# Kernel optimization log

Hardware: AMD Instinct MI355X
Metric: run time of the kernel (lower is better)

The kernel has to match this reference:

```python
import jax, jax.numpy as jnp
import numpy as np


def _gru_cell(x, h, W_ih, W_hh, b_ih, b_hh):
    # torch.nn.GRUCell math. x: [T,H], h: [T,H]; W_*: [3H,H]; b_*: [3H]
    gi = x @ W_ih.T + b_ih          # [T,3H]
    gh = h @ W_hh.T + b_hh          # [T,3H]
    i_r, i_z, i_n = jnp.split(gi, 3, axis=-1)
    h_r, h_z, h_n = jnp.split(gh, 3, axis=-1)
    r = jax.nn.sigmoid(i_r + h_r)
    z = jax.nn.sigmoid(i_z + h_z)
    n = jnp.tanh(i_n + r * h_n)
    return (1.0 - z) * n + z * h


def setup_inputs() -> dict:
    key = jax.random.key(0)
    ks = jax.random.split(key, 7)
    S, T, H = 65536, 8192, 1024
    bound = 1.0 / np.sqrt(H)  # torch GRUCell init scale
    return {
        "speaker_memory": jax.random.normal(ks[0], (S, H), dtype=jnp.float32),
        "speaker_ids": jax.random.randint(ks[1], (T,), 0, S, dtype=jnp.int32),
        "edu_reps": jax.random.normal(ks[2], (T, H), dtype=jnp.float32),
        "W_ih": jax.random.uniform(ks[3], (3 * H, H), jnp.float32, -bound, bound),
        "W_hh": jax.random.uniform(ks[4], (3 * H, H), jnp.float32, -bound, bound),
        "b_ih": jax.random.uniform(ks[5], (3 * H,), jnp.float32, -bound, bound),
        "b_hh": jax.random.uniform(ks[6], (3 * H,), jnp.float32, -bound, bound),
    }


def reference(speaker_memory, speaker_ids, edu_reps, W_ih, W_hh, b_ih, b_hh):
    # The torch loop reads h from the ORIGINAL speaker_memory for every step,
    # so all T GRU updates are independent; for duplicate speaker ids the last
    S, H = speaker_memory.shape
    T = speaker_ids.shape[0]
    h = speaker_memory[speaker_ids]                      # [T,H] gather
    new_h = _gru_cell(edu_reps, h, W_ih, W_hh, b_ih, b_hh)  # [T,H]
    # last occurrence position of each speaker id (int min for untouched ids)
    last_pos = jax.ops.segment_max(jnp.arange(T), speaker_ids, num_segments=S)
    touched = last_pos >= 0                              # [S]
    gathered = new_h[jnp.clip(last_pos, 0, T - 1)]       # [S,H]
    return jnp.where(touched[:, None], gathered, speaker_memory)
```

## Files before the change

kernel.cpp:

```cpp
#include <hip/hip_runtime.h>
#include <hip/hip_bf16.h>
#include <stdint.h>
#include <stddef.h>

typedef short short8 __attribute__((ext_vector_type(8)));
typedef float f32x4 __attribute__((ext_vector_type(4)));

#define SROWS 65536
#define TROWS 8192
#define HDIM  1024
#define KDIM  2048
#define NDIM  4096
#define NT    (KDIM / 64)

__device__ __forceinline__ unsigned short f2bf(float f) {
  union { float f; uint32_t u; } v; v.f = f;
  uint32_t u = v.u;
  uint32_t r = (u + 0x7FFFu + ((u >> 16) & 1u)) >> 16;
  return (unsigned short)r;
}

__device__ __forceinline__ float fast_sigmoid(float x) {
  return __builtin_amdgcn_rcpf(1.0f + __builtin_amdgcn_exp2f(-1.44269504f * x));
}
__device__ __forceinline__ float fast_tanh(float x) {
  return 1.0f - 2.0f * __builtin_amdgcn_rcpf(1.0f + __builtin_amdgcn_exp2f(2.88539008f * x));
}


__global__ __launch_bounds__(256) void k_initlp(int* lp) {
  int i = blockIdx.x * 256 + threadIdx.x;
  if (i < SROWS) lp[i] = -1;
}

__global__ __launch_bounds__(256) void k_lp(const int* __restrict__ sid, int* lp) {
  int i = blockIdx.x * 256 + threadIdx.x;
  if (i < TROWS) atomicMax(&lp[sid[i]], i);
}

__global__ __launch_bounds__(256) void k_flags(const int* __restrict__ lp,
                                               unsigned long long* __restrict__ flagb) {
  int i = blockIdx.x * 256 + threadIdx.x;
  unsigned long long m = __ballot(lp[i] < 0);
  if ((threadIdx.x & 63) == 0) flagb[i >> 6] = m;
}

__global__ __launch_bounds__(256) void k_bias(const float* __restrict__ bih,
                                              const float* __restrict__ bhh,
                                              float* __restrict__ btab) {
  int j = blockIdx.x * 256 + threadIdx.x;
  if (j < HDIM) {
    btab[4*j+0] = bih[j] + bhh[j];
    btab[4*j+1] = bih[j+HDIM] + bhh[j+HDIM];
    btab[4*j+2] = bih[j+2*HDIM];
    btab[4*j+3] = bhh[j+2*HDIM];
  }
}

__global__ __launch_bounds__(256) void k_build_A(const float* __restrict__ edu,
                                                 const float* __restrict__ mem,
                                                 const int* __restrict__ sid,
                                                 unsigned short* __restrict__ Ac) {
  const int idx = blockIdx.x * 256 + threadIdx.x;
  const int t  = idx >> 8;
  const int k0 = (idx & 255) << 3;
  const float* src;
  if (k0 < HDIM) src = edu + (size_t)t * HDIM + k0;
  else           src = mem + (size_t)sid[t] * HDIM + (k0 - HDIM);
  f32x4 f0 = *(const f32x4*)src;
  f32x4 f1 = *(const f32x4*)(src + 4);
  short8 v;
  v[0]=(short)f2bf(f0[0]); v[1]=(short)f2bf(f0[1]); v[2]=(short)f2bf(f0[2]); v[3]=(short)f2bf(f0[3]);
  v[4]=(short)f2bf(f1[0]); v[5]=(short)f2bf(f1[1]); v[6]=(short)f2bf(f1[2]); v[7]=(short)f2bf(f1[3]);
  *(short8*)(Ac + (size_t)idx * 8) = v;
}

__global__ __launch_bounds__(256) void k_build_B(const float* __restrict__ Wih,
                                                 const float* __restrict__ Whh,
                                                 unsigned short* __restrict__ Bc) {
  const int idx = blockIdx.x * 256 + threadIdx.x;
  const int c  = idx >> 8;
  const int k0 = (idx & 255) << 3;
  const int j  = c >> 2;
  const int g  = c & 3;
  const float* src = nullptr;
  if (g == 0)      src = (k0 < HDIM) ? Wih + (size_t)j * HDIM + k0
                                     : Whh + (size_t)j * HDIM + (k0 - HDIM);
  else if (g == 1) src = (k0 < HDIM) ? Wih + (size_t)(j + HDIM) * HDIM + k0
                                     : Whh + (size_t)(j + HDIM) * HDIM + (k0 - HDIM);
  else if (g == 2) { if (k0 < HDIM)  src = Wih + (size_t)(j + 2*HDIM) * HDIM + k0; }
  else             { if (k0 >= HDIM) src = Whh + (size_t)(j + 2*HDIM) * HDIM + (k0 - HDIM); }
  short8 v = (short8)0;
  if (src) {
    f32x4 f0 = *(const f32x4*)src;
    f32x4 f1 = *(const f32x4*)(src + 4);
    v[0]=(short)f2bf(f0[0]); v[1]=(short)f2bf(f0[1]); v[2]=(short)f2bf(f0[2]); v[3]=(short)f2bf(f0[3]);
    v[4]=(short)f2bf(f1[0]); v[5]=(short)f2bf(f1[1]); v[6]=(short)f2bf(f1[2]); v[7]=(short)f2bf(f1[3]);
  }
  *(short8*)(Bc + (size_t)idx * 8) = v;
}


#define FENCE() asm volatile("" ::: "memory")
#define BAR()   __builtin_amdgcn_s_barrier()
#define LGKM0() asm volatile("s_waitcnt lgkmcnt(0)" ::: "memory")
#define VM(N)   asm volatile("s_waitcnt vmcnt(" #N ")" ::: "memory")

#define STAGE(p0, p1, ldsoff)                                                              \
  __builtin_amdgcn_global_load_lds((const __attribute__((address_space(1))) void*)(p0),   \
      (__attribute__((address_space(3))) void*)(smem + (ldsoff) + w * 1024), 16, 0, 0);    \
  __builtin_amdgcn_global_load_lds((const __attribute__((address_space(1))) void*)(p1),   \
      (__attribute__((address_space(3))) void*)(smem + (ldsoff) + 8192 + w * 1024), 16, 0, 0);

#define LDF(base, frag, koff) (*(const short8*)(smem + (base) + (size_t)(frag) * 2048 + (koff)))

__global__ __launch_bounds__(512, 2)
void k_gru8(const unsigned short* __restrict__ Ac,
            const unsigned short* __restrict__ Bc,
            const float* __restrict__ mem,
            const int* __restrict__ sid,
            const int* __restrict__ lp,
            const unsigned long long* __restrict__ flagb,
            const float* __restrict__ btab,
            float* __restrict__ out) {
  extern __shared__ char smem[];

  const int tid  = threadIdx.x;
  const int lane = tid & 63;
  const int w    = tid >> 6;
  const int wm   = w >> 2;
  const int wn   = w & 3;
  const int l15  = lane & 15;
  const int l4   = lane >> 4;

  const int bid = blockIdx.x;
  const int swz = (bid & 7) * 64 + (bid >> 3);
  const int t0  = (swz >> 4) * 256;
  const int c0  = (swz & 15) * 256;

  const int srow0 = tid >> 3;
  const int srow1 = 64 + srow0;
  const int scol  = ((tid & 7) * 8) ^ (((tid >> 3) & 7) << 3);

  const unsigned short* pA0r0 = Ac + (size_t)(t0 +       srow0) * KDIM + scol;
  const unsigned short* pA0r1 = Ac + (size_t)(t0 +       srow1) * KDIM + scol;
  const unsigned short* pA1r0 = Ac + (size_t)(t0 + 128 + srow0) * KDIM + scol;
  const unsigned short* pA1r1 = Ac + (size_t)(t0 + 128 + srow1) * KDIM + scol;
  const unsigned short* pB0r0 = Bc + (size_t)(c0 +       srow0) * KDIM + scol;
  const unsigned short* pB0r1 = Bc + (size_t)(c0 +       srow1) * KDIM + scol;
  const unsigned short* pB1r0 = Bc + (size_t)(c0 + 128 + srow0) * KDIM + scol;
  const unsigned short* pB1r1 = Bc + (size_t)(c0 + 128 + srow1) * KDIM + scol;

  const int rsw = (l15 & 7) << 4;
  const size_t foff0 = (size_t)l15 * 128 + ((l4 * 16)      ^ rsw);
  const size_t foff1 = (size_t)l15 * 128 + ((64 + l4 * 16) ^ rsw);

  f32x4 acc[8][4];
#pragma unroll
  for (int i = 0; i < 8; i++)
#pragma unroll
    for (int j = 0; j < 4; j++) acc[i][j] = (f32x4){0.f, 0.f, 0.f, 0.f};

  const int cbase = bid << 7;
  const unsigned long long fw0 = flagb[bid * 2];
  const unsigned long long fw1 = flagb[bid * 2 + 1];
  const int ccp  = tid >> 8;
  const int ccol = (tid & 255) << 2;
  f32x4 cpX0, cpX1, cpY0, cpY1;
  bool  vX0 = false, vX1 = false, vY0 = false, vY1 = false;
  int   sX0 = 0, sX1 = 0, sY0 = 0, sY1 = 0;

  STAGE(pA0r0, pA0r1, 0);
  STAGE(pA1r0, pA1r1, 16384);
  STAGE(pB0r0, pB0r1, 32768);
  STAGE(pB1r0, pB1r1, 49152);
  STAGE(pB0r0 + 64, pB0r1 + 64, 65536 + 32768);
  STAGE(pB1r0 + 64, pB1r1 + 64, 65536 + 49152);
  VM(4);
  FENCE(); BAR();

  for (int t = 0; t < NT; ++t) {
    const int cur = t & 1, nxt = cur ^ 1;
    const size_t abase = (size_t)cur * 65536 + (size_t)wm * 16384;
    const size_t bbase = (size_t)cur * 65536 + 32768 + (size_t)(wn >> 1) * 16384
                       + (size_t)(wn & 1) * 8192;
    const int kt1 = (t + 1 < NT) ? t + 1 : NT - 1;
    const int kt2 = (t + 2 < NT) ? t + 2 : NT - 1;

    short8 bf[4][2];
#pragma unroll
    for (int q = 0; q < 4; q++) {
      const int m0 = 2 * q;
      if (q == 0) {
#pragma unroll
        for (int n = 0; n < 4; n++) {
          bf[n][0] = LDF(bbase, n, foff0);
          bf[n][1] = LDF(bbase, n, foff1);
        }
      }
      short8 af[2][2];
      af[0][0] = LDF(abase, m0,     foff0);
      af[0][1] = LDF(abase, m0,     foff1);
      af[1][0] = LDF(abase, m0 + 1, foff0);
      af[1][1] = LDF(abase, m0 + 1, foff1);

      if (q == 0)      { STAGE(pA0r0 + kt1 * 64, pA0r1 + kt1 * 64, (size_t)nxt * 65536); }
      else if (q == 1) { STAGE(pA1r0 + kt1 * 64, pA1r1 + kt1 * 64, (size_t)nxt * 65536 + 16384); }
      else if (q == 2) { STAGE(pB0r0 + kt2 * 64, pB0r1 + kt2 * 64, (size_t)cur * 65536 + 32768); }
      else             { STAGE(pB1r0 + kt2 * 64, pB1r1 + kt2 * 64, (size_t)cur * 65536 + 49152); }

      FENCE(); BAR();
      LGKM0();
      __builtin_amdgcn_s_setprio(1);
#pragma unroll
      for (int i = 0; i < 2; i++)
#pragma unroll
        for (int n = 0; n < 4; n++) {
          acc[m0 + i][n] = __builtin_amdgcn_mfma_f32_16x16x32_bf16(af[i][0], bf[n][0], acc[m0 + i][n], 0, 0, 0);
          acc[m0 + i][n] = __builtin_amdgcn_mfma_f32_16x16x32_bf16(af[i][1], bf[n][1], acc[m0 + i][n], 0, 0, 0);
        }
      __builtin_amdgcn_s_setprio(0);
      if (q == 3) {
        VM(4);
        const int rr0 = 4 * t + ccp, rr1 = rr0 + 2;
        const unsigned long long fwt = (t < 16) ? fw0 : fw1;
        const bool nv0 = (fwt >> (rr0 & 63)) & 1ull;
        const bool nv1 = (fwt >> (rr1 & 63)) & 1ull;
        if ((t & 1) == 0) {
          if (vY0) __builtin_nontemporal_store(cpY0, (f32x4*)&out[(size_t)sY0 * HDIM + ccol]);
          if (vY1) __builtin_nontemporal_store(cpY1, (f32x4*)&out[(size_t)sY1 * HDIM + ccol]);
          vX0 = nv0; vX1 = nv1; sX0 = cbase + rr0; sX1 = cbase + rr1;
          if (vX0) cpX0 = __builtin_nontemporal_load((const f32x4*)&mem[(size_t)sX0 * HDIM + ccol]);
          if (vX1) cpX1 = __builtin_nontemporal_load((const f32x4*)&mem[(size_t)sX1 * HDIM + ccol]);
        } else {
          if (vX0) __builtin_nontemporal_store(cpX0, (f32x4*)&out[(size_t)sX0 * HDIM + ccol]);
          if (vX1) __builtin_nontemporal_store(cpX1, (f32x4*)&out[(size_t)sX1 * HDIM + ccol]);
          vY0 = nv0; vY1 = nv1; sY0 = cbase + rr0; sY1 = cbase + rr1;
          if (vY0) cpY0 = __builtin_nontemporal_load((const f32x4*)&mem[(size_t)sY0 * HDIM + ccol]);
          if (vY1) cpY1 = __builtin_nontemporal_load((const f32x4*)&mem[(size_t)sY1 * HDIM + ccol]);
        }
      }
      FENCE(); BAR();
    }
  }

  VM(0);
  if (vY0) __builtin_nontemporal_store(cpY0, (f32x4*)&out[(size_t)sY0 * HDIM + ccol]);
  if (vY1) __builtin_nontemporal_store(cpY1, (f32x4*)&out[(size_t)sY1 * HDIM + ccol]);
  __syncthreads();
  float* epi = (float*)smem;
  const int jfirst = ((c0 + wn * 64) >> 2) + l4 * 4;

#pragma unroll
  for (int mf = 0; mf < 8; mf++) {
#pragma unroll
    for (int nf = 0; nf < 4; nf++)
#pragma unroll
      for (int r = 0; r < 4; r++)
        epi[w * 1088 + (l4 * 4 + r) * 68 + nf * 16 + l15] = acc[mf][nf][r];
    __syncthreads();

    const int trow = t0 + wm * 128 + mf * 16 + l15;
    const int s    = sid[trow];
    const bool wr  = (lp[s] == trow);

    f32x4 q[4];
#pragma unroll
    for (int jj = 0; jj < 4; jj++)
      q[jj] = *(const f32x4*)&epi[w * 1088 + l15 * 68 + l4 * 16 + jj * 4];

    f32x4 hv = *(const f32x4*)&mem[(size_t)s * HDIM + jfirst];
    f32x4 o;
#pragma unroll
    for (int jj = 0; jj < 4; jj++) {
      const int j = jfirst + jj;
      f32x4 bt = *(const f32x4*)&btab[4 * j];
      float rr = fast_sigmoid(q[jj][0] + bt[0]);
      float zz = fast_sigmoid(q[jj][1] + bt[1]);
      float nn = fast_tanh(q[jj][2] + bt[2] + rr * (q[jj][3] + bt[3]));
      o[jj] = (1.0f - zz) * nn + zz * hv[jj];
    }
    if (wr) __builtin_nontemporal_store(o, (f32x4*)&out[(size_t)s * HDIM + jfirst]);
    __syncthreads();
  }
}


extern "C" void kernel_launch(void* const* d_in, const int* in_sizes, int n_in,
                              void* d_out, int out_size, void* d_ws, size_t ws_size,
                              hipStream_t stream) {
  const float* mem = (const float*)d_in[0];
  const int*   sid = (const int*)d_in[1];
  const float* edu = (const float*)d_in[2];
  const float* Wih = (const float*)d_in[3];
  const float* Whh = (const float*)d_in[4];
  const float* bih = (const float*)d_in[5];
  const float* bhh = (const float*)d_in[6];
  float* out = (float*)d_out;

  char* p = (char*)d_ws;
  unsigned short* Ac = (unsigned short*)p; p += (size_t)TROWS * KDIM * 2;
  unsigned short* Bc = (unsigned short*)p; p += (size_t)NDIM * KDIM * 2;
  int*   lp   = (int*)p;   p += (size_t)SROWS * 4;
  float* btab = (float*)p; p += (size_t)HDIM * 4 * 4;
  unsigned long long* flagb = (unsigned long long*)p; p += (size_t)(SROWS / 64) * 8;

  hipFuncSetAttribute((const void*)k_gru8, hipFuncAttributeMaxDynamicSharedMemorySize, 131072);

  hipLaunchKernelGGL(k_initlp, dim3(SROWS / 256), dim3(256), 0, stream, lp);
  hipLaunchKernelGGL(k_lp, dim3(TROWS / 256), dim3(256), 0, stream, sid, lp);
  hipLaunchKernelGGL(k_flags, dim3(SROWS / 256), dim3(256), 0, stream, lp, flagb);
  hipLaunchKernelGGL(k_bias, dim3(4), dim3(256), 0, stream, bih, bhh, btab);
  hipLaunchKernelGGL(k_build_A, dim3((TROWS * KDIM / 8) / 256), dim3(256), 0, stream, edu, mem, sid, Ac);
  hipLaunchKernelGGL(k_build_B, dim3((NDIM * KDIM / 8) / 256), dim3(256), 0, stream, Wih, Whh, Bc);
  hipLaunchKernelGGL(k_gru8, dim3(512), dim3(512), 131072, stream,
                     Ac, Bc, mem, sid, lp, flagb, btab, out);
}
```

Before: 230.7 us.

## Drop zero-padded halves of n-gate weights by splitting B into rz and n panels

```diff
diff --git a/kernel.cpp b/kernel.cpp
--- a/kernel.cpp
+++ b/kernel.cpp
@@ -10,8 +10,8 @@
 #define TROWS 8192
 #define HDIM  1024
 #define KDIM  2048
-#define NDIM  4096
-#define NT    (KDIM / 64)
+#define NT    32
+#define BUF   57344
 
 __device__ __forceinline__ unsigned short f2bf(float f) {
   union { float f; uint32_t u; } v; v.f = f;
@@ -75,29 +75,33 @@
   *(short8*)(Ac + (size_t)idx * 8) = v;
 }
 
-__global__ __launch_bounds__(256) void k_build_B(const float* __restrict__ Wih,
-                                                 const float* __restrict__ Whh,
-                                                 unsigned short* __restrict__ Bc) {
+__global__ __launch_bounds__(256) void k_build_B2(const float* __restrict__ Wih,
+                                                  const float* __restrict__ Whh,
+                                                  unsigned short* __restrict__ Brz,
+                                                  unsigned short* __restrict__ Bn) {
   const int idx = blockIdx.x * 256 + threadIdx.x;
   const int c  = idx >> 8;
   const int k0 = (idx & 255) << 3;
-  const int j  = c >> 2;
-  const int g  = c & 3;
-  const float* src = nullptr;
-  if (g == 0)      src = (k0 < HDIM) ? Wih + (size_t)j * HDIM + k0
-                                     : Whh + (size_t)j * HDIM + (k0 - HDIM);
-  else if (g == 1) src = (k0 < HDIM) ? Wih + (size_t)(j + HDIM) * HDIM + k0
-                                     : Whh + (size_t)(j + HDIM) * HDIM + (k0 - HDIM);
-  else if (g == 2) { if (k0 < HDIM)  src = Wih + (size_t)(j + 2*HDIM) * HDIM + k0; }
-  else             { if (k0 >= HDIM) src = Whh + (size_t)(j + 2*HDIM) * HDIM + (k0 - HDIM); }
-  short8 v = (short8)0;
-  if (src) {
-    f32x4 f0 = *(const f32x4*)src;
-    f32x4 f1 = *(const f32x4*)(src + 4);
-    v[0]=(short)f2bf(f0[0]); v[1]=(short)f2bf(f0[1]); v[2]=(short)f2bf(f0[2]); v[3]=(short)f2bf(f0[3]);
-    v[4]=(short)f2bf(f1[0]); v[5]=(short)f2bf(f1[1]); v[6]=(short)f2bf(f1[2]); v[7]=(short)f2bf(f1[3]);
-  }
-  *(short8*)(Bc + (size_t)idx * 8) = v;
+  const float* src;
+  unsigned short* dst;
+  if (c < 2048) {
+    const int j = c >> 1, g = c & 1;
+    const int row = j + g * 1024;
+    src = (k0 < HDIM) ? Wih + (size_t)row * HDIM + k0
+                      : Whh + (size_t)row * HDIM + (k0 - HDIM);
+    dst = Brz + (size_t)c * KDIM + k0;
+  } else {
+    const int j = c - 2048;
+    src = (k0 < HDIM) ? Wih + (size_t)(j + 2*HDIM) * HDIM + k0
+                      : Whh + (size_t)(j + 2*HDIM) * HDIM + (k0 - HDIM);
+    dst = Bn + (size_t)j * KDIM + k0;
+  }
+  f32x4 f0 = *(const f32x4*)src;
+  f32x4 f1 = *(const f32x4*)(src + 4);
+  short8 v;
+  v[0]=(short)f2bf(f0[0]); v[1]=(short)f2bf(f0[1]); v[2]=(short)f2bf(f0[2]); v[3]=(short)f2bf(f0[3]);
+  v[4]=(short)f2bf(f1[0]); v[5]=(short)f2bf(f1[1]); v[6]=(short)f2bf(f1[2]); v[7]=(short)f2bf(f1[3]);
+  *(short8*)dst = v;
 }
 
 
@@ -112,11 +116,86 @@
   __builtin_amdgcn_global_load_lds((const __attribute__((address_space(1))) void*)(p1),   \
       (__attribute__((address_space(3))) void*)(smem + (ldsoff) + 8192 + w * 1024), 16, 0, 0);
 
+#define STAGE1(p0, ldsoff)                                                                 \
+  __builtin_amdgcn_global_load_lds((const __attribute__((address_space(1))) void*)(p0),   \
+      (__attribute__((address_space(3))) void*)(smem + (ldsoff) + w * 1024), 16, 0, 0);
+
 #define LDF(base, frag, koff) (*(const short8*)(smem + (base) + (size_t)(frag) * 2048 + (koff)))
+
+#define MF(a, b, c) __builtin_amdgcn_mfma_f32_16x16x32_bf16(a, b, c, 0, 0, 0)
+
+#define PHASE(m0, STAGE_STMT, TAIL, ACCN)                                     \
+  {                                                                           \
+    short8 af0a = LDF(abase, (m0),     foff0);                                \
+    short8 af0b = LDF(abase, (m0),     foff1);                                \
+    short8 af1a = LDF(abase, (m0) + 1, foff0);                                \
+    short8 af1b = LDF(abase, (m0) + 1, foff1);                                \
+    STAGE_STMT;                                                               \
+    FENCE(); BAR();                                                           \
+    LGKM0();                                                                  \
+    __builtin_amdgcn_s_setprio(1);                                            \
+    acc_rz[(m0)][0]   = MF(af0a, bf[0][0], acc_rz[(m0)][0]);                  \
+    acc_rz[(m0)][0]   = MF(af0b, bf[0][1], acc_rz[(m0)][0]);                  \
+    acc_rz[(m0)][1]   = MF(af0a, bf[1][0], acc_rz[(m0)][1]);                  \
+    acc_rz[(m0)][1]   = MF(af0b, bf[1][1], acc_rz[(m0)][1]);                  \
+    ACCN[(m0)]        = MF(af0a, bf[2][0], ACCN[(m0)]);                       \
+    ACCN[(m0)]        = MF(af0b, bf[2][1], ACCN[(m0)]);                       \
+    acc_rz[(m0)+1][0] = MF(af1a, bf[0][0], acc_rz[(m0)+1][0]);                \
+    acc_rz[(m0)+1][0] = MF(af1b, bf[0][1], acc_rz[(m0)+1][0]);                \
+    acc_rz[(m0)+1][1] = MF(af1a, bf[1][0], acc_rz[(m0)+1][1]);                \
+    acc_rz[(m0)+1][1] = MF(af1b, bf[1][1], acc_rz[(m0)+1][1]);                \
+    ACCN[(m0)+1]      = MF(af1a, bf[2][0], ACCN[(m0)+1]);                     \
+    ACCN[(m0)+1]      = MF(af1b, bf[2][1], ACCN[(m0)+1]);                     \
+    __builtin_amdgcn_s_setprio(0);                                            \
+    TAIL;                                                                     \
+    FENCE(); BAR();                                                           \
+  }
+
+#define COPY_TAIL                                                             \
+  {                                                                           \
+    VM(3);                                                                    \
+    const int rr0 = 4 * t + ccp, rr1 = rr0 + 2;                               \
+    const unsigned long long fwt = (t < 16) ? fw0 : fw1;                      \
+    const bool nv0 = (fwt >> (rr0 & 63)) & 1ull;                              \
+    const bool nv1 = (fwt >> (rr1 & 63)) & 1ull;                              \
+    if ((t & 1) == 0) {                                                       \
+      if (vY0) __builtin_nontemporal_store(cpY0, (f32x4*)&out[(size_t)sY0 * HDIM + ccol]); \
+      if (vY1) __builtin_nontemporal_store(cpY1, (f32x4*)&out[(size_t)sY1 * HDIM + ccol]); \
+      vX0 = nv0; vX1 = nv1; sX0 = cbase + rr0; sX1 = cbase + rr1;             \
+      if (vX0) cpX0 = __builtin_nontemporal_load((const f32x4*)&mem[(size_t)sX0 * HDIM + ccol]); \
+      if (vX1) cpX1 = __builtin_nontemporal_load((const f32x4*)&mem[(size_t)sX1 * HDIM + ccol]); \
+    } else {                                                                  \
+      if (vX0) __builtin_nontemporal_store(cpX0, (f32x4*)&out[(size_t)sX0 * HDIM + ccol]); \
+      if (vX1) __builtin_nontemporal_store(cpX1, (f32x4*)&out[(size_t)sX1 * HDIM + ccol]); \
+      vY0 = nv0; vY1 = nv1; sY0 = cbase + rr0; sY1 = cbase + rr1;             \
+      if (vY0) cpY0 = __builtin_nontemporal_load((const f32x4*)&mem[(size_t)sY0 * HDIM + ccol]); \
+      if (vY1) cpY1 = __builtin_nontemporal_load((const f32x4*)&mem[(size_t)sY1 * HDIM + ccol]); \
+    }                                                                         \
+  }
+
+#define TILE_BODY(ACCN)                                                       \
+  {                                                                           \
+    const int cur = t & 1, nxt = cur ^ 1;                                     \
+    const size_t buf = (size_t)cur * BUF, nbuf = (size_t)nxt * BUF;           \
+    const size_t abase  = buf + (size_t)wm * 16384;                           \
+    const size_t rzbase = buf + 32768 + (size_t)wn * 4096;                    \
+    const size_t nbase  = buf + 49152 + (size_t)wn * 2048;                    \
+    const int kt1 = (t + 1 < NT) ? t + 1 : NT - 1;                            \
+    const int kt2 = (t + 2 < NT) ? t + 2 : NT - 1;                            \
+    short8 bf[3][2];                                                          \
+    bf[0][0] = LDF(rzbase, 0, foff0); bf[0][1] = LDF(rzbase, 0, foff1);       \
+    bf[1][0] = LDF(rzbase, 1, foff0); bf[1][1] = LDF(rzbase, 1, foff1);       \
+    bf[2][0] = LDF(nbase,  0, foff0); bf[2][1] = LDF(nbase,  0, foff1);       \
+    PHASE(0, STAGE(pA0r0 + kt1 * 64, pA0r1 + kt1 * 64, nbuf), ;, ACCN)        \
+    PHASE(2, STAGE(pA1r0 + kt1 * 64, pA1r1 + kt1 * 64, nbuf + 16384), ;, ACCN)\
+    PHASE(4, STAGE(pRZ0 + kt2 * 64, pRZ1 + kt2 * 64, buf + 32768), ;, ACCN)   \
+    PHASE(6, STAGE1(pN + kt2 * 64, buf + 49152), COPY_TAIL, ACCN)             \
+  }
 
 __global__ __launch_bounds__(512, 2)
 void k_gru8(const unsigned short* __restrict__ Ac,
-            const unsigned short* __restrict__ Bc,
+            const unsigned short* __restrict__ Brz,
+            const unsigned short* __restrict__ Bn,
             const float* __restrict__ mem,
             const int* __restrict__ sid,
             const int* __restrict__ lp,
@@ -136,7 +215,8 @@
   const int bid = blockIdx.x;
   const int swz = (bid & 7) * 64 + (bid >> 3);
   const int t0  = (swz >> 4) * 256;
-  const int c0  = (swz & 15) * 256;
+  const int j0  = (swz & 15) * 64;
+  const int rz0 = j0 * 2;
 
   const int srow0 = tid >> 3;
   const int srow1 = 64 + srow0;
@@ -146,20 +226,22 @@
   const unsigned short* pA0r1 = Ac + (size_t)(t0 +       srow1) * KDIM + scol;
   const unsigned short* pA1r0 = Ac + (size_t)(t0 + 128 + srow0) * KDIM + scol;
   const unsigned short* pA1r1 = Ac + (size_t)(t0 + 128 + srow1) * KDIM + scol;
-  const unsigned short* pB0r0 = Bc + (size_t)(c0 +       srow0) * KDIM + scol;
-  const unsigned short* pB0r1 = Bc + (size_t)(c0 +       srow1) * KDIM + scol;
-  const unsigned short* pB1r0 = Bc + (size_t)(c0 + 128 + srow0) * KDIM + scol;
-  const unsigned short* pB1r1 = Bc + (size_t)(c0 + 128 + srow1) * KDIM + scol;
+  const unsigned short* pRZ0  = Brz + (size_t)(rz0 + srow0) * KDIM + scol;
+  const unsigned short* pRZ1  = Brz + (size_t)(rz0 + srow1) * KDIM + scol;
+  const unsigned short* pN    = Bn  + (size_t)(j0  + srow0) * KDIM + scol;
 
   const int rsw = (l15 & 7) << 4;
   const size_t foff0 = (size_t)l15 * 128 + ((l4 * 16)      ^ rsw);
   const size_t foff1 = (size_t)l15 * 128 + ((64 + l4 * 16) ^ rsw);
 
-  f32x4 acc[8][4];
-#pragma unroll
-  for (int i = 0; i < 8; i++)
-#pragma unroll
-    for (int j = 0; j < 4; j++) acc[i][j] = (f32x4){0.f, 0.f, 0.f, 0.f};
+  f32x4 acc_rz[8][2], acc_nlo[8], acc_nhi[8];
+#pragma unroll
+  for (int i = 0; i < 8; i++) {
+    acc_rz[i][0] = (f32x4){0.f,0.f,0.f,0.f};
+    acc_rz[i][1] = (f32x4){0.f,0.f,0.f,0.f};
+    acc_nlo[i]   = (f32x4){0.f,0.f,0.f,0.f};
+    acc_nhi[i]   = (f32x4){0.f,0.f,0.f,0.f};
+  }
 
   const int cbase = bid << 7;
   const unsigned long long fw0 = flagb[bid * 2];
@@ -172,92 +254,35 @@
 
   STAGE(pA0r0, pA0r1, 0);
   STAGE(pA1r0, pA1r1, 16384);
-  STAGE(pB0r0, pB0r1, 32768);
-  STAGE(pB1r0, pB1r1, 49152);
-  STAGE(pB0r0 + 64, pB0r1 + 64, 65536 + 32768);
-  STAGE(pB1r0 + 64, pB1r1 + 64, 65536 + 49152);
-  VM(4);
+  STAGE(pRZ0, pRZ1, 32768);
+  STAGE1(pN, 49152);
+  STAGE(pRZ0 + 64, pRZ1 + 64, BUF + 32768);
+  STAGE1(pN + 64, BUF + 49152);
+  VM(3);
   FENCE(); BAR();
 
-  for (int t = 0; t < NT; ++t) {
-    const int cur = t & 1, nxt = cur ^ 1;
-    const size_t abase = (size_t)cur * 65536 + (size_t)wm * 16384;
-    const size_t bbase = (size_t)cur * 65536 + 32768 + (size_t)(wn >> 1) * 16384
-                       + (size_t)(wn & 1) * 8192;
-    const int kt1 = (t + 1 < NT) ? t + 1 : NT - 1;
-    const int kt2 = (t + 2 < NT) ? t + 2 : NT - 1;
-
-    short8 bf[4][2];
-#pragma unroll
-    for (int q = 0; q < 4; q++) {
-      const int m0 = 2 * q;
-      if (q == 0) {
-#pragma unroll
-        for (int n = 0; n < 4; n++) {
-          bf[n][0] = LDF(bbase, n, foff0);
-          bf[n][1] = LDF(bbase, n, foff1);
-        }
-      }
-      short8 af[2][2];
-      af[0][0] = LDF(abase, m0,     foff0);
-      af[0][1] = LDF(abase, m0,     foff1);
-      af[1][0] = LDF(abase, m0 + 1, foff0);
-      af[1][1] = LDF(abase, m0 + 1, foff1);
-
-      if (q == 0)      { STAGE(pA0r0 + kt1 * 64, pA0r1 + kt1 * 64, (size_t)nxt * 65536); }
-      else if (q == 1) { STAGE(pA1r0 + kt1 * 64, pA1r1 + kt1 * 64, (size_t)nxt * 65536 + 16384); }
-      else if (q == 2) { STAGE(pB0r0 + kt2 * 64, pB0r1 + kt2 * 64, (size_t)cur * 65536 + 32768); }
-      else             { STAGE(pB1r0 + kt2 * 64, pB1r1 + kt2 * 64, (size_t)cur * 65536 + 49152); }
-
-      FENCE(); BAR();
-      LGKM0();
-      __builtin_amdgcn_s_setprio(1);
-#pragma unroll
-      for (int i = 0; i < 2; i++)
-#pragma unroll
-        for (int n = 0; n < 4; n++) {
-          acc[m0 + i][n] = __builtin_amdgcn_mfma_f32_16x16x32_bf16(af[i][0], bf[n][0], acc[m0 + i][n], 0, 0, 0);
-          acc[m0 + i][n] = __builtin_amdgcn_mfma_f32_16x16x32_bf16(af[i][1], bf[n][1], acc[m0 + i][n], 0, 0, 0);
-        }
-      __builtin_amdgcn_s_setprio(0);
-      if (q == 3) {
-        VM(4);
-        const int rr0 = 4 * t + ccp, rr1 = rr0 + 2;
-        const unsigned long long fwt = (t < 16) ? fw0 : fw1;
-        const bool nv0 = (fwt >> (rr0 & 63)) & 1ull;
-        const bool nv1 = (fwt >> (rr1 & 63)) & 1ull;
-        if ((t & 1) == 0) {
-          if (vY0) __builtin_nontemporal_store(cpY0, (f32x4*)&out[(size_t)sY0 * HDIM + ccol]);
-          if (vY1) __builtin_nontemporal_store(cpY1, (f32x4*)&out[(size_t)sY1 * HDIM + ccol]);
-          vX0 = nv0; vX1 = nv1; sX0 = cbase + rr0; sX1 = cbase + rr1;
-          if (vX0) cpX0 = __builtin_nontemporal_load((const f32x4*)&mem[(size_t)sX0 * HDIM + ccol]);
-          if (vX1) cpX1 = __builtin_nontemporal_load((const f32x4*)&mem[(size_t)sX1 * HDIM + ccol]);
-        } else {
-          if (vX0) __builtin_nontemporal_store(cpX0, (f32x4*)&out[(size_t)sX0 * HDIM + ccol]);
-          if (vX1) __builtin_nontemporal_store(cpX1, (f32x4*)&out[(size_t)sX1 * HDIM + ccol]);
-          vY0 = nv0; vY1 = nv1; sY0 = cbase + rr0; sY1 = cbase + rr1;
-          if (vY0) cpY0 = __builtin_nontemporal_load((const f32x4*)&mem[(size_t)sY0 * HDIM + ccol]);
-          if (vY1) cpY1 = __builtin_nontemporal_load((const f32x4*)&mem[(size_t)sY1 * HDIM + ccol]);
-        }
-      }
-      FENCE(); BAR();
-    }
-  }
+  for (int t = 0; t < 16; ++t) TILE_BODY(acc_nlo)
+  for (int t = 16; t < NT; ++t) TILE_BODY(acc_nhi)
 
   VM(0);
   if (vY0) __builtin_nontemporal_store(cpY0, (f32x4*)&out[(size_t)sY0 * HDIM + ccol]);
   if (vY1) __builtin_nontemporal_store(cpY1, (f32x4*)&out[(size_t)sY1 * HDIM + ccol]);
   __syncthreads();
   float* epi = (float*)smem;
-  const int jfirst = ((c0 + wn * 64) >> 2) + l4 * 4;
+  const int jfirst = j0 + wn * 16 + l4 * 4;
 
 #pragma unroll
   for (int mf = 0; mf < 8; mf++) {
 #pragma unroll
-    for (int nf = 0; nf < 4; nf++)
+    for (int f = 0; f < 2; f++)
 #pragma unroll
       for (int r = 0; r < 4; r++)
-        epi[w * 1088 + (l4 * 4 + r) * 68 + nf * 16 + l15] = acc[mf][nf][r];
+        epi[w * 1088 + (l4 * 4 + r) * 68 + (f * 8 + (l15 >> 1)) * 4 + (l15 & 1)] = acc_rz[mf][f][r];
+#pragma unroll
+    for (int r = 0; r < 4; r++) {
+      epi[w * 1088 + (l4 * 4 + r) * 68 + l15 * 4 + 2] = acc_nlo[mf][r];
+      epi[w * 1088 + (l4 * 4 + r) * 68 + l15 * 4 + 3] = acc_nhi[mf][r];
+    }
     __syncthreads();
 
     const int trow = t0 + wm * 128 + mf * 16 + l15;
@@ -299,20 +324,21 @@
   float* out = (float*)d_out;
 
   char* p = (char*)d_ws;
-  unsigned short* Ac = (unsigned short*)p; p += (size_t)TROWS * KDIM * 2;
-  unsigned short* Bc = (unsigned short*)p; p += (size_t)NDIM * KDIM * 2;
+  unsigned short* Ac  = (unsigned short*)p; p += (size_t)TROWS * KDIM * 2;
+  unsigned short* Brz = (unsigned short*)p; p += (size_t)2048 * KDIM * 2;
+  unsigned short* Bn  = (unsigned short*)p; p += (size_t)1024 * KDIM * 2;
   int*   lp   = (int*)p;   p += (size_t)SROWS * 4;
   float* btab = (float*)p; p += (size_t)HDIM * 4 * 4;
   unsigned long long* flagb = (unsigned long long*)p; p += (size_t)(SROWS / 64) * 8;
 
-  hipFuncSetAttribute((const void*)k_gru8, hipFuncAttributeMaxDynamicSharedMemorySize, 131072);
+  hipFuncSetAttribute((const void*)k_gru8, hipFuncAttributeMaxDynamicSharedMemorySize, 2 * BUF);
 
   hipLaunchKernelGGL(k_initlp, dim3(SROWS / 256), dim3(256), 0, stream, lp);
   hipLaunchKernelGGL(k_lp, dim3(TROWS / 256), dim3(256), 0, stream, sid, lp);
   hipLaunchKernelGGL(k_flags, dim3(SROWS / 256), dim3(256), 0, stream, lp, flagb);
   hipLaunchKernelGGL(k_bias, dim3(4), dim3(256), 0, stream, bih, bhh, btab);
   hipLaunchKernelGGL(k_build_A, dim3((TROWS * KDIM / 8) / 256), dim3(256), 0, stream, edu, mem, sid, Ac);
-  hipLaunchKernelGGL(k_build_B, dim3((NDIM * KDIM / 8) / 256), dim3(256), 0, stream, Wih, Whh, Bc);
-  hipLaunchKernelGGL(k_gru8, dim3(512), dim3(512), 131072, stream,
-                     Ac, Bc, mem, sid, lp, flagb, btab, out);
-}
+  hipLaunchKernelGGL(k_build_B2, dim3(3072), dim3(256), 0, stream, Wih, Whh, Brz, Bn);
+  hipLaunchKernelGGL(k_gru8, dim3(512), dim3(512), 2 * BUF, stream,
+                     Ac, Brz, Bn, mem, sid, lp, flagb, btab, out);
+}
```

After: 207.4 us. -10.1%, faster.
